# Kernel tuning notes

Hardware: AMD Instinct MI355X
Metric: run time of the kernel (lower is better)

The kernel has to match this reference:

```python
import jax, jax.numpy as jnp
import numpy as np

B, T, I, H, O = 64, 2000, 2, 512, 1
DT, TAU = 10.0, 100.0
EXCIT = 0.8
SIG_REC, SIG_IN = 0.01, 0.01
ALPHA = DT / TAU
IN_SCALE = float(np.sqrt(2.0 * (DT / TAU) * SIG_IN ** 2))
REC_SCALE = float(np.sqrt(2.0 * (TAU / DT) * SIG_REC ** 2))


def setup_inputs() -> dict:
    key = jax.random.key(0)
    ks = jax.random.split(key, 8)
    xav = lambda k, shp, gain: gain * np.sqrt(2.0 / (shp[0] + shp[1])) * jax.random.normal(k, shp, jnp.float32)
    return {
        "i_stim": jax.random.normal(ks[0], (B, T), jnp.float32),
        "i_cc": jax.random.normal(ks[1], (B, T), jnp.float32),
        "hidden": jnp.zeros((B, H), jnp.float32),
        "w_ih": xav(ks[2], (H, I), 1.0),
        "b_ih": jnp.zeros((H,), jnp.float32),
        "w_hh": jax.nn.relu(xav(ks[3], (H, H), 0.1)),  # init applies relu to w_hh
        "b_hh": jnp.zeros((H,), jnp.float32),
        "w_ho": xav(ks[4], (O, H), 1.0),
        "b_ho": jnp.zeros((O,), jnp.float32),
    }


def reference(i_stim, i_cc, hidden, w_ih, b_ih, w_hh, b_hh, w_ho, b_ho):
    ei = jnp.where(jnp.arange(H) < int(EXCIT * H), 1.0, -1.0).astype(w_hh.dtype)
    w_hh_ei = jnp.abs(w_hh * (1.0 - jnp.eye(H, dtype=w_hh.dtype))) * ei  # [H,H], time-invariant

    inputs = jnp.stack([i_stim, i_cc], axis=-1).transpose(1, 0, 2)  # [T,B,2]
    nk = jax.random.key(42)
    n_in = jax.random.normal(jax.random.fold_in(nk, 0), (T, B, I), inputs.dtype)
    n_rec = jax.random.normal(jax.random.fold_in(nk, 1), (T, B, H), hidden.dtype)

    def step(h, xs):
        x_t, ni, nr = xs
        cur = jax.nn.relu(x_t + IN_SCALE * ni)  # training=True path
        hid_in = cur @ w_ih.T  # [B,H]; note b_ih is never added (faithful to source)
        hid_hid = jax.nn.relu(h) @ w_hh_ei.T + b_hh + REC_SCALE * nr
        h_new = h + (-h + hid_in + hid_hid) * ALPHA
        out = jax.nn.relu(h_new) @ w_ho.T + b_ho  # [B,O]
        return h_new, (out, h_new)

    _, (outs, hids) = jax.lax.scan(step, hidden, (inputs, n_in, n_rec))
    return outs.transpose(1, 0, 2), hids.transpose(1, 0, 2)  # [B,T,O], [B,T,H]
```

## Files before the change

### kernel.cpp

```cpp
#include <hip/hip_runtime.h>
#include <stdint.h>
#include <math.h>

#define HH   512
#define BB   64
#define TT   2000
#define NEXC 409
#define SLICE  128
#define NBLK   (BB * 4)

constexpr float ALPHA_F     = 0.1f;
constexpr float IN_SCALE_F  = (float)4.4721359549995794e-03;
constexpr float REC_SCALE_F = (float)4.4721359549995794e-02;
constexpr float SQRT2_F     = 1.41421356237309515f;
constexpr float U_LO        = -0x1.fffffep-1f;

struct U2 { uint32_t a, b; };

__host__ __device__ constexpr uint32_t rotl32(uint32_t x, int d) {
  return (x << d) | (x >> (32 - d));
}

__host__ __device__ constexpr U2 tf2x32(uint32_t k0, uint32_t k1,
                                        uint32_t x0, uint32_t x1) {
  uint32_t ks[3] = {k0, k1, k0 ^ k1 ^ 0x1BD11BDAu};
  const int R[2][4] = {{13, 15, 26, 6}, {17, 29, 16, 24}};
  x0 += ks[0]; x1 += ks[1];
  for (int g = 0; g < 5; ++g) {
    const int* r = R[g & 1];
    for (int i = 0; i < 4; ++i) { x0 += x1; x1 = rotl32(x1, r[i]); x1 ^= x0; }
    x0 += ks[(g + 1) % 3];
    x1 += ks[(g + 2) % 3] + (uint32_t)(g + 1);
  }
  return U2{x0, x1};
}

constexpr U2 KIN_  = tf2x32(0u, 42u, 0u, 0u);
constexpr U2 KREC_ = tf2x32(0u, 42u, 0u, 1u);
constexpr uint32_t KIN0 = KIN_.a,  KIN1 = KIN_.b;
constexpr uint32_t KRC0 = KREC_.a, KRC1 = KREC_.b;

__device__ __forceinline__ float jax_normal(uint32_t k0, uint32_t k1, uint32_t idx) {
  U2 o = tf2x32(k0, k1, 0u, idx);
  uint32_t bits = o.a ^ o.b;
  float f = __uint_as_float((bits >> 9) | 0x3f800000u) - 1.0f;
  float u = fmaxf(U_LO, f * 2.0f + U_LO);
  float w = -log1pf(-u * u);
  float p;
  if (w < 5.0f) {
    w = w - 2.5f;
    p =             2.81022636e-08f;
    p = fmaf(p, w,  3.43273939e-07f);
    p = fmaf(p, w, -3.5233877e-06f);
    p = fmaf(p, w, -4.39150654e-06f);
    p = fmaf(p, w,  0.00021858087f);
    p = fmaf(p, w, -0.00125372503f);
    p = fmaf(p, w, -0.00417768164f);
    p = fmaf(p, w,  0.246640727f);
    p = fmaf(p, w,  1.50140941f);
  } else {
    w = sqrtf(w) - 3.0f;
    p =            -0.000200214257f;
    p = fmaf(p, w,  0.000100950558f);
    p = fmaf(p, w,  0.00134934322f);
    p = fmaf(p, w, -0.00367342844f);
    p = fmaf(p, w,  0.00573950773f);
    p = fmaf(p, w, -0.0076224613f);
    p = fmaf(p, w,  0.00943887047f);
    p = fmaf(p, w,  1.00167406f);
    p = fmaf(p, w,  2.83297682f);
  }
  return SQRT2_F * (p * u);
}

#define PUB_WORDS (2 * BB * HH)
#define PUB_BYTES (PUB_WORDS * 8)

__global__ __launch_bounds__(512, 2)
void zrnn_main(const float* __restrict__ i_stim, const float* __restrict__ i_cc,
               const float* __restrict__ hidden0,
               const float* __restrict__ w_ih, const float* __restrict__ w_hh,
               const float* __restrict__ b_hh,
               const float* __restrict__ w_ho, const float* __restrict__ b_ho,
               float* __restrict__ outs, float* __restrict__ hids,
               uint64_t* __restrict__ pub) {
  const int bid  = blockIdx.x;
  const int low3 = bid & 7;
  const int q    = bid >> 3;
  const int s    = q & 3;
  const int b    = ((q >> 2) << 3) + low3;
  const int tid  = threadIdx.x;
  const int lane = tid & 63;
  const int wv   = tid >> 6;

  __shared__ float stim_s[TT];
  __shared__ float cc_s[TT];
  __shared__ float red[8][SLICE];
  __shared__ float rloc[SLICE];
  __shared__ float nbuf[4][SLICE];
  __shared__ float nin_s[4][2];
  __shared__ float obuf[8];

  for (int idx = tid; idx < TT; idx += 512) {
    stim_s[idx] = i_stim[b * TT + idx];
    cc_s[idx]   = i_cc[b * TT + idx];
  }

  const int jA = s * SLICE + lane;
  const int jB = jA + 64;
  const int i0 = wv * 64;
  float wA[64], wB[64];
  #pragma unroll
  for (int k4 = 0; k4 < 16; ++k4) {
    float4 a4 = *reinterpret_cast<const float4*>(&w_hh[jA * HH + i0 + k4 * 4]);
    float4 b4 = *reinterpret_cast<const float4*>(&w_hh[jB * HH + i0 + k4 * 4]);
    const float av[4] = {a4.x, a4.y, a4.z, a4.w};
    const float bv[4] = {b4.x, b4.y, b4.z, b4.w};
    #pragma unroll
    for (int c = 0; c < 4; ++c) {
      const int i = i0 + k4 * 4 + c;
      float va = (i == jA) ? 0.0f : fabsf(av[c]);
      float vb = (i == jB) ? 0.0f : fabsf(bv[c]);
      wA[k4 * 4 + c] = (i < NEXC) ? va : -va;
      wB[k4 * 4 + c] = (i < NEXC) ? vb : -vb;
    }
  }

  float h = 0.0f, wih0 = 0.0f, wih1 = 0.0f, bhh = 0.0f;
  const int jown = s * SLICE + tid;
  if (tid < SLICE) {
    h    = hidden0[b * HH + jown];
    wih0 = w_ih[jown * 2 + 0];
    wih1 = w_ih[jown * 2 + 1];
    bhh  = b_hh[jown];
  }
  float who_f = 0.0f, bho = 0.0f;
  if (s == 0) { who_f = w_ho[tid]; bho = b_ho[0]; }

  float rv = fmaxf(hidden0[b * HH + tid], 0.0f);

  {
    const int tp = tid >> 7;
    const int jn = tid & 127;
    nbuf[tp][jn] = jax_normal(KRC0, KRC1,
        (uint32_t)tp * (uint32_t)(BB * HH) + (uint32_t)(b * HH + s * SLICE + jn));
    if (tid < 8) {
      const int tp2  = tid >> 1;
      const int slot = tid & 1;
      nin_s[tp2][slot] = jax_normal(KIN0, KIN1,
          (uint32_t)(tp2 * (BB * 2) + b * 2 + slot));
    }
  }

  const int  ownLo     = s * SLICE;
  const bool isOwnLane = (tid >= ownLo) && (tid < ownLo + SLICE);
  uint64_t* pub_b0 = pub + (size_t)b * HH;
  uint64_t* pub_b1 = pub + (size_t)(BB + b) * HH;
  float* __restrict__ hid_out = hids + (size_t)b * TT * HH;

  __syncthreads();

  for (int t = 0; t < TT; ++t) {
    if (s == 0 && t > 0) {
      float v = rv * who_f;
      #pragma unroll
      for (int off = 32; off > 0; off >>= 1) v += __shfl_down(v, off);
      if (lane == 0) obuf[wv] = v;
    }

    float accA = 0.0f, accB = 0.0f;
    #pragma unroll
    for (int k = 0; k < 64; ++k) {
      float rk = __uint_as_float(__builtin_amdgcn_readlane(__float_as_uint(rv), k));
      accA = fmaf(rk, wA[k], accA);
      accB = fmaf(rk, wB[k], accB);
    }
    red[wv][lane]      = accA;
    red[wv][64 + lane] = accB;
    __syncthreads();

    uint64_t* pub_t = (t & 1) ? pub_b1 : pub_b0;

    if (tid < SLICE) {
      float acc = red[0][tid];
      #pragma unroll
      for (int w = 1; w < 8; ++w) acc += red[w][tid];
      float nr = nbuf[t & 3][tid];
      float hid_hid = acc + bhh + REC_SCALE_F * nr;
      float ni0 = nin_s[t & 3][0];
      float ni1 = nin_s[t & 3][1];
      float cur0 = fmaxf(stim_s[t] + IN_SCALE_F * ni0, 0.0f);
      float cur1 = fmaxf(cc_s[t]   + IN_SCALE_F * ni1, 0.0f);
      float hid_in = cur0 * wih0 + cur1 * wih1;
      h = h + (-h + hid_in + hid_hid) * ALPHA_F;
      __builtin_nontemporal_store(h, hid_out + (size_t)t * HH + jown);
      float r = fmaxf(h, 0.0f);
      uint64_t wd = ((uint64_t)(uint32_t)(t + 1) << 32) |
                    (uint64_t)__float_as_uint(r);
      __hip_atomic_store(&pub_t[jown], wd, __ATOMIC_RELAXED,
                         __HIP_MEMORY_SCOPE_AGENT);
      rloc[tid] = r;
      if (s == 0 && tid == 0 && t > 0) {
        float p = ((obuf[0] + obuf[1]) + (obuf[2] + obuf[3])) +
                  ((obuf[4] + obuf[5]) + (obuf[6] + obuf[7]));
        outs[b * TT + (t - 1)] = p + bho;
      }
    }
    __syncthreads();

    if ((t & 3) == 3 && t + 1 < TT) {
      const int tp = t + 1 + (tid >> 7);
      if (tp < TT) {
        const int jn = tid & 127;
        nbuf[tp & 3][jn] = jax_normal(KRC0, KRC1,
            (uint32_t)tp * (uint32_t)(BB * HH) + (uint32_t)(b * HH + s * SLICE + jn));
      }
      if (tid < 8) {
        const int tp2  = t + 1 + (tid >> 1);
        const int slot = tid & 1;
        if (tp2 < TT)
          nin_s[tp2 & 3][slot] = jax_normal(KIN0, KIN1,
              (uint32_t)(tp2 * (BB * 2) + b * 2 + slot));
      }
    }

    if (isOwnLane) {
      rv = rloc[tid - ownLo];
    } else {
      const uint32_t tagw = (uint32_t)(t + 1);
      uint64_t w = __hip_atomic_load(&pub_t[tid], __ATOMIC_RELAXED,
                                     __HIP_MEMORY_SCOPE_AGENT);
      while ((uint32_t)(w >> 32) != tagw) {
        __builtin_amdgcn_s_sleep(1);
        w = __hip_atomic_load(&pub_t[tid], __ATOMIC_RELAXED,
                              __HIP_MEMORY_SCOPE_AGENT);
      }
      rv = __uint_as_float((uint32_t)w);
    }
  }

  if (s == 0) {
    float v = rv * who_f;
    #pragma unroll
    for (int off = 32; off > 0; off >>= 1) v += __shfl_down(v, off);
    if (lane == 0) obuf[wv] = v;
    __syncthreads();
    if (tid == 0) {
      float p = ((obuf[0] + obuf[1]) + (obuf[2] + obuf[3])) +
                ((obuf[4] + obuf[5]) + (obuf[6] + obuf[7]));
      outs[b * TT + (TT - 1)] = p + bho;
    }
  }
}

extern "C" void kernel_launch(void* const* d_in, const int* in_sizes, int n_in,
                              void* d_out, int out_size, void* d_ws, size_t ws_size,
                              hipStream_t stream) {
  const float* i_stim = (const float*)d_in[0];
  const float* i_cc   = (const float*)d_in[1];
  const float* hidden = (const float*)d_in[2];
  const float* w_ih   = (const float*)d_in[3];
  const float* w_hh   = (const float*)d_in[5];
  const float* b_hh   = (const float*)d_in[6];
  const float* w_ho   = (const float*)d_in[7];
  const float* b_ho   = (const float*)d_in[8];

  float* outs   = (float*)d_out;
  float* hids   = (float*)d_out + (size_t)BB * TT;
  uint64_t* pub = (uint64_t*)d_ws;

  hipMemsetAsync(pub, 0, PUB_BYTES, stream);

  void* args[] = {(void*)&i_stim, (void*)&i_cc, (void*)&hidden, (void*)&w_ih,
                  (void*)&w_hh, (void*)&b_hh, (void*)&w_ho, (void*)&b_ho,
                  (void*)&outs, (void*)&hids, (void*)&pub};
  hipLaunchCooperativeKernel((const void*)zrnn_main, dim3(NBLK), dim3(512),
                             args, 0, stream);
}
```

Baseline: 3.998 ms.

## Remove per-step second barrier via double-buffered reduction and owner-lane state

The shared reduction buffer becomes double-buffered by step parity. The threads whose index matches the block's own hidden slice now do the update and keep their relu state in a register, which removes the rloc staging buffer and the second __syncthreads per timestep. Noise generation is spread across steps, with each owner lane refilling its own ring slot right after use instead of in a burst every fourth step. The output-projection reduction now rotates across the four slice blocks, and the spin-wait busy-polls a few times before sleeping. This cuts barrier and serialization latency on the recurrent critical path, at the cost of more shared memory, more register use and harder-to-check ordering between shared buffers.

```diff
diff --git a/kernel.cpp b/kernel.cpp
--- a/kernel.cpp
+++ b/kernel.cpp
@@ -93,10 +93,13 @@
   const int lane = tid & 63;
   const int wv   = tid >> 6;
 
+  const int  ownLo = s * SLICE;
+  const bool isOwn = (tid >= ownLo) && (tid < ownLo + SLICE);
+  const int  jloc  = tid - ownLo;
+
   __shared__ float stim_s[TT];
   __shared__ float cc_s[TT];
-  __shared__ float red[8][SLICE];
-  __shared__ float rloc[SLICE];
+  __shared__ float red[2][8][SLICE];
   __shared__ float nbuf[4][SLICE];
   __shared__ float nin_s[4][2];
   __shared__ float obuf[8];
@@ -106,7 +109,7 @@
     cc_s[idx]   = i_cc[b * TT + idx];
   }
 
-  const int jA = s * SLICE + lane;
+  const int jA = ownLo + lane;
   const int jB = jA + 64;
   const int i0 = wv * 64;
   float wA[64], wB[64];
@@ -127,33 +130,27 @@
   }
 
   float h = 0.0f, wih0 = 0.0f, wih1 = 0.0f, bhh = 0.0f;
-  const int jown = s * SLICE + tid;
-  if (tid < SLICE) {
-    h    = hidden0[b * HH + jown];
-    wih0 = w_ih[jown * 2 + 0];
-    wih1 = w_ih[jown * 2 + 1];
-    bhh  = b_hh[jown];
-  }
-  float who_f = 0.0f, bho = 0.0f;
-  if (s == 0) { who_f = w_ho[tid]; bho = b_ho[0]; }
+  if (isOwn) {
+    h    = hidden0[b * HH + tid];
+    wih0 = w_ih[tid * 2 + 0];
+    wih1 = w_ih[tid * 2 + 1];
+    bhh  = b_hh[tid];
+  }
+  const float who_f = w_ho[tid];
+  const float bho   = b_ho[0];
 
   float rv = fmaxf(hidden0[b * HH + tid], 0.0f);
 
-  {
-    const int tp = tid >> 7;
-    const int jn = tid & 127;
-    nbuf[tp][jn] = jax_normal(KRC0, KRC1,
-        (uint32_t)tp * (uint32_t)(BB * HH) + (uint32_t)(b * HH + s * SLICE + jn));
-    if (tid < 8) {
-      const int tp2  = tid >> 1;
-      const int slot = tid & 1;
-      nin_s[tp2][slot] = jax_normal(KIN0, KIN1,
-          (uint32_t)(tp2 * (BB * 2) + b * 2 + slot));
-    }
-  }
-
-  const int  ownLo     = s * SLICE;
-  const bool isOwnLane = (tid >= ownLo) && (tid < ownLo + SLICE);
+  if (isOwn) {
+    #pragma unroll
+    for (int tp = 0; tp < 4; ++tp)
+      nbuf[tp][jloc] = jax_normal(KRC0, KRC1,
+          (uint32_t)tp * (uint32_t)(BB * HH) + (uint32_t)(b * HH + tid));
+    if (jloc < 8)
+      nin_s[jloc >> 1][jloc & 1] = jax_normal(KIN0, KIN1,
+          (uint32_t)((jloc >> 1) * (BB * 2) + b * 2 + (jloc & 1)));
+  }
+
   uint64_t* pub_b0 = pub + (size_t)b * HH;
   uint64_t* pub_b1 = pub + (size_t)(BB + b) * HH;
   float* __restrict__ hid_out = hids + (size_t)b * TT * HH;
@@ -161,13 +158,24 @@
   __syncthreads();
 
   for (int t = 0; t < TT; ++t) {
-    if (s == 0 && t > 0) {
+    const int par = t & 1;
+
+    if (t > 0 && s == ((t - 1) & 3)) {
       float v = rv * who_f;
       #pragma unroll
       for (int off = 32; off > 0; off >>= 1) v += __shfl_down(v, off);
       if (lane == 0) obuf[wv] = v;
     }
 
+    float nr = 0.0f, ni0 = 0.0f, ni1 = 0.0f, x0 = 0.0f, x1 = 0.0f;
+    if (isOwn) {
+      nr  = nbuf[t & 3][jloc];
+      ni0 = nin_s[t & 3][0];
+      ni1 = nin_s[t & 3][1];
+      x0  = stim_s[t];
+      x1  = cc_s[t];
+    }
+
     float accA = 0.0f, accB = 0.0f;
     #pragma unroll
     for (int k = 0; k < 64; ++k) {
@@ -175,80 +183,71 @@
       accA = fmaf(rk, wA[k], accA);
       accB = fmaf(rk, wB[k], accB);
     }
-    red[wv][lane]      = accA;
-    red[wv][64 + lane] = accB;
+    red[par][wv][lane]      = accA;
+    red[par][wv][64 + lane] = accB;
     __syncthreads();
 
-    uint64_t* pub_t = (t & 1) ? pub_b1 : pub_b0;
-
-    if (tid < SLICE) {
-      float acc = red[0][tid];
+    uint64_t* pub_t = par ? pub_b1 : pub_b0;
+
+    if (isOwn) {
+      float acc = red[par][0][jloc];
       #pragma unroll
-      for (int w = 1; w < 8; ++w) acc += red[w][tid];
-      float nr = nbuf[t & 3][tid];
+      for (int w = 1; w < 8; ++w) acc += red[par][w][jloc];
       float hid_hid = acc + bhh + REC_SCALE_F * nr;
-      float ni0 = nin_s[t & 3][0];
-      float ni1 = nin_s[t & 3][1];
-      float cur0 = fmaxf(stim_s[t] + IN_SCALE_F * ni0, 0.0f);
-      float cur1 = fmaxf(cc_s[t]   + IN_SCALE_F * ni1, 0.0f);
+      float cur0 = fmaxf(x0 + IN_SCALE_F * ni0, 0.0f);
+      float cur1 = fmaxf(x1 + IN_SCALE_F * ni1, 0.0f);
       float hid_in = cur0 * wih0 + cur1 * wih1;
       h = h + (-h + hid_in + hid_hid) * ALPHA_F;
-      __builtin_nontemporal_store(h, hid_out + (size_t)t * HH + jown);
       float r = fmaxf(h, 0.0f);
       uint64_t wd = ((uint64_t)(uint32_t)(t + 1) << 32) |
                     (uint64_t)__float_as_uint(r);
-      __hip_atomic_store(&pub_t[jown], wd, __ATOMIC_RELAXED,
+      __hip_atomic_store(&pub_t[tid], wd, __ATOMIC_RELAXED,
                          __HIP_MEMORY_SCOPE_AGENT);
-      rloc[tid] = r;
-      if (s == 0 && tid == 0 && t > 0) {
-        float p = ((obuf[0] + obuf[1]) + (obuf[2] + obuf[3])) +
-                  ((obuf[4] + obuf[5]) + (obuf[6] + obuf[7]));
-        outs[b * TT + (t - 1)] = p + bho;
+      rv = r;
+      __builtin_nontemporal_store(h, hid_out + (size_t)t * HH + tid);
+
+      if (tid == ownLo && t > 0 && s == ((t - 1) & 3)) {
+        float psum = ((obuf[0] + obuf[1]) + (obuf[2] + obuf[3])) +
+                     ((obuf[4] + obuf[5]) + (obuf[6] + obuf[7]));
+        outs[b * TT + (t - 1)] = psum + bho;
       }
-    }
-    __syncthreads();
-
-    if ((t & 3) == 3 && t + 1 < TT) {
-      const int tp = t + 1 + (tid >> 7);
-      if (tp < TT) {
-        const int jn = tid & 127;
-        nbuf[tp & 3][jn] = jax_normal(KRC0, KRC1,
-            (uint32_t)tp * (uint32_t)(BB * HH) + (uint32_t)(b * HH + s * SLICE + jn));
+
+      if (t + 4 < TT) {
+        nbuf[t & 3][jloc] = jax_normal(KRC0, KRC1,
+            (uint32_t)(t + 4) * (uint32_t)(BB * HH) + (uint32_t)(b * HH + tid));
+        if (jloc < 2)
+          nin_s[t & 3][jloc] = jax_normal(KIN0, KIN1,
+              (uint32_t)((t + 4) * (BB * 2) + b * 2 + jloc));
       }
-      if (tid < 8) {
-        const int tp2  = t + 1 + (tid >> 1);
-        const int slot = tid & 1;
-        if (tp2 < TT)
-          nin_s[tp2 & 3][slot] = jax_normal(KIN0, KIN1,
-              (uint32_t)(tp2 * (BB * 2) + b * 2 + slot));
-      }
-    }
-
-    if (isOwnLane) {
-      rv = rloc[tid - ownLo];
     } else {
       const uint32_t tagw = (uint32_t)(t + 1);
       uint64_t w = __hip_atomic_load(&pub_t[tid], __ATOMIC_RELAXED,
                                      __HIP_MEMORY_SCOPE_AGENT);
-      while ((uint32_t)(w >> 32) != tagw) {
-        __builtin_amdgcn_s_sleep(1);
-        w = __hip_atomic_load(&pub_t[tid], __ATOMIC_RELAXED,
-                              __HIP_MEMORY_SCOPE_AGENT);
+      if ((uint32_t)(w >> 32) != tagw) {
+        uint64_t w2 = __hip_atomic_load(&pub_t[tid], __ATOMIC_RELAXED,
+                                        __HIP_MEMORY_SCOPE_AGENT);
+        int spins = 0;
+        while ((uint32_t)(w >> 32) != tagw) {
+          w = w2;
+          if (++spins > 16) __builtin_amdgcn_s_sleep(1);
+          w2 = __hip_atomic_load(&pub_t[tid], __ATOMIC_RELAXED,
+                                 __HIP_MEMORY_SCOPE_AGENT);
+        }
       }
       rv = __uint_as_float((uint32_t)w);
     }
   }
 
-  if (s == 0) {
+  if (s == ((TT - 1) & 3)) {
     float v = rv * who_f;
     #pragma unroll
     for (int off = 32; off > 0; off >>= 1) v += __shfl_down(v, off);
     if (lane == 0) obuf[wv] = v;
     __syncthreads();
-    if (tid == 0) {
-      float p = ((obuf[0] + obuf[1]) + (obuf[2] + obuf[3])) +
-                ((obuf[4] + obuf[5]) + (obuf[6] + obuf[7]));
-      outs[b * TT + (TT - 1)] = p + bho;
+    if (tid == ownLo) {
+      float psum = ((obuf[0] + obuf[1]) + (obuf[2] + obuf[3])) +
+                   ((obuf[4] + obuf[5]) + (obuf[6] + obuf[7]));
+      outs[b * TT + (TT - 1)] = psum + bho;
     }
   }
 }
```

Result: slower. 4.230 ms (+5.8%).
